# Kernel tuning notes

Measured on AMD Instinct MI355X. Metric: run time of the kernel, lower is better.

## Reference

```python
import jax, jax.numpy as jnp
import numpy as np

B, N, D, H, O = 256, 1024, 512, 2048, 512


def setup_inputs() -> dict:
    key = jax.random.key(0)
    ks = jax.random.split(key, 6)
    x = jax.random.normal(ks[0], (B, N, D), dtype=jnp.float32)
    # binary float mask [B,N,1]; ensure every set has >=1 unpadded element
    mask = (jax.random.uniform(ks[1], (B, N, 1)) < 0.9).astype(jnp.float32)
    mask = mask.at[:, :1, :].set(1.0)
    # per-row (4B rows after stat-concat) unpadded counts in [1, N]
    unpadded = jax.random.randint(ks[2], (4 * B, 1), 1, N + 1).astype(jnp.float32)
    W1 = jax.random.normal(ks[3], (D, H), dtype=jnp.float32) * (1.0 / np.sqrt(D))
    b1 = jnp.zeros((H,), jnp.float32)
    W2 = jax.random.normal(ks[4], (H, O), dtype=jnp.float32) * (1.0 / np.sqrt(H))
    b2 = jnp.zeros((O,), jnp.float32)
    return dict(x=x, mask=mask, unpadded=unpadded, W1=W1, b1=b1, W2=W2, b2=b2)


def reference(x, mask, unpadded, W1, b1, W2, b2):
    # x: [B,N,D], mask: [B,N,1] (0/1 float)
    neg_inf = jnp.float32(-jnp.inf)
    cnt = mask.sum(axis=1)                              # [B,1]
    mean = (x * mask).sum(axis=1) / cnt                 # [B,D]
    agg_max = jnp.where(mask > 0, x, neg_inf).max(axis=1)   # [B,D]
    agg_min = -jnp.where(mask > 0, -x, neg_inf).max(axis=1) # [B,D]
    var = (jnp.square(x - mean[:, None, :]) * mask).sum(axis=1) / cnt
    std = jnp.sqrt(var)                                 # [B,D]
    aggr = jnp.concatenate([mean, agg_max, agg_min, std], axis=0)  # [4B,D]
    # faithful to source: delta = sum(unpadded)/unpadded.shape[1] + 1 (scalar)
    delta = unpadded.sum() / unpadded.shape[1] + 1.0
    logu = jnp.log(unpadded + 1.0)                      # [4B,1]
    amplification = aggr * (logu / delta)
    attenuation = aggr * (delta / logu)
    scale_concat = jnp.concatenate([aggr, amplification, attenuation], axis=0)  # [12B,D]
    h = jax.nn.relu(scale_concat @ W1 + b1)
    return h @ W2 + b2                                  # [12B,O]
```

## Files before the change

kernel.cpp:

```cpp
#include <hip/hip_runtime.h>
#include <hip/hip_bf16.h>
#include <math.h>
#include <stdint.h>

#define B_  256
#define N_  1024
#define D_  512
#define H_  2048
#define O_  512
#define M4  (4 * B_)
#define M12 (12 * B_)
#define NCH 8

typedef __attribute__((ext_vector_type(8))) short short8;
typedef __attribute__((ext_vector_type(4))) float f32x4;
typedef unsigned short ushort_t;

__device__ inline uint32_t pkbf(float a, float b) {
    union { __hip_bfloat162 h; uint32_t u; } cv;
    cv.h = __float22bfloat162_rn(float2{a, b});
    return cv.u;
}
__device__ inline ushort_t f2bf(float f) {
    union { float f; uint32_t u; } v; v.f = f;
    uint32_t r = v.u + 0x7FFFu + ((v.u >> 16) & 1u);
    return (ushort_t)(r >> 16);
}

__device__ inline void load_lds16(const void* g, void* l) {
    typedef const __attribute__((address_space(1))) uint32_t* gp_t;
    typedef __attribute__((address_space(3))) uint32_t* lp_t;
    __builtin_amdgcn_global_load_lds((gp_t)(uintptr_t)g, (lp_t)(uint32_t)(uintptr_t)l,
                                     16, 0, 0);
}

__device__ __forceinline__ void agg_core(const float* __restrict__ x,
                                         const float* __restrict__ mask,
                                         float* __restrict__ part,
                                         float* __restrict__ cntp,
                                         int id, int t) {
    const int b    = id >> 2;
    const int c    = id & 3;
    const int half = t >> 7;
    const int d4   = (t & 127) << 2;
    const float* base = x + ((size_t)b * N_ + (size_t)c * 256) * D_ + d4;
    const float* mp   = mask + (size_t)b * N_ + (size_t)c * 256;

    f32x4 sum = {0.f,0.f,0.f,0.f}, sq = {0.f,0.f,0.f,0.f};
    f32x4 mx = {-INFINITY,-INFINITY,-INFINITY,-INFINITY};
    f32x4 mn = { INFINITY, INFINITY, INFINITY, INFINITY};
    float cnt = 0.f;

    #pragma unroll 8
    for (int n = half; n < 256; n += 2) {
        float m = mp[n];
        f32x4 v = __builtin_nontemporal_load((const f32x4*)(base + (size_t)n * D_));
        sum.x = fmaf(v.x, m, sum.x); sum.y = fmaf(v.y, m, sum.y);
        sum.z = fmaf(v.z, m, sum.z); sum.w = fmaf(v.w, m, sum.w);
        sq.x  = fmaf(v.x * v.x, m, sq.x); sq.y = fmaf(v.y * v.y, m, sq.y);
        sq.z  = fmaf(v.z * v.z, m, sq.z); sq.w = fmaf(v.w * v.w, m, sq.w);
        cnt  += m;
        bool um = m > 0.f;
        mx.x = um ? fmaxf(mx.x, v.x) : mx.x; mx.y = um ? fmaxf(mx.y, v.y) : mx.y;
        mx.z = um ? fmaxf(mx.z, v.z) : mx.z; mx.w = um ? fmaxf(mx.w, v.w) : mx.w;
        mn.x = um ? fminf(mn.x, v.x) : mn.x; mn.y = um ? fminf(mn.y, v.y) : mn.y;
        mn.z = um ? fminf(mn.z, v.z) : mn.z; mn.w = um ? fminf(mn.w, v.w) : mn.w;
    }

    const int ch = c * 2 + half;
    const size_t SS = (size_t)B_ * NCH * D_;
    const size_t pi = ((size_t)(b * NCH + ch)) * D_ + d4;
    *(f32x4*)(part + 0 * SS + pi) = sum;
    *(f32x4*)(part + 1 * SS + pi) = sq;
    *(f32x4*)(part + 2 * SS + pi) = mx;
    *(f32x4*)(part + 3 * SS + pi) = mn;
    if ((t & 127) == 0) cntp[b * NCH + ch] = cnt;
}

__device__ void conv_tile(const float* __restrict__ in, ushort_t* __restrict__ out,
                          int R, int C, int bx, int by, float* tile) {
    const int t  = threadIdx.x;
    const int r0 = by << 5;
    const int c0 = bx << 5;
    const int tr = t >> 3;
    const int tc = (t & 7) << 2;

    float4 v = *(const float4*)(in + (size_t)(r0 + tr) * C + c0 + tc);
    tile[tr * 33 + tc + 0] = v.x; tile[tr * 33 + tc + 1] = v.y;
    tile[tr * 33 + tc + 2] = v.z; tile[tr * 33 + tc + 3] = v.w;
    __syncthreads();

    union { uint32_t u[2]; ushort4 us; } o;
    o.u[0] = pkbf(tile[(tc + 0) * 33 + tr], tile[(tc + 1) * 33 + tr]);
    o.u[1] = pkbf(tile[(tc + 2) * 33 + tr], tile[(tc + 3) * 33 + tr]);
    *(ushort4*)(out + (size_t)(c0 + tr) * R + r0 + tc) = o.us;
}

__global__ __launch_bounds__(256) void k1_mega(const float* __restrict__ x,
                                               const float* __restrict__ mask,
                                               const float* __restrict__ W1,
                                               const float* __restrict__ W2,
                                               const float* __restrict__ unpadded,
                                               float* __restrict__ part,
                                               float* __restrict__ cntp,
                                               ushort_t* __restrict__ W1t,
                                               ushort_t* __restrict__ W2t,
                                               float* __restrict__ scale) {
    __shared__ float smem[32 * 33];
    const int id = blockIdx.x;
    const int t  = threadIdx.x;

    if (id < 1024) {
        agg_core(x, mask, part, cntp, id, t);
    } else if (id < 2048) {
        const int tid = id - 1024;
        conv_tile(W1, W1t, D_, H_, tid & 63, tid >> 6, smem);
    } else if (id < 3072) {
        const int tid = id - 2048;
        conv_tile(W2, W2t, H_, O_, tid & 15, tid >> 4, smem);
    } else {
        float4 u4 = *(const float4*)(unpadded + t * 4);
        smem[t] = u4.x + u4.y + u4.z + u4.w;
        __syncthreads();
        for (int s = 128; s > 0; s >>= 1) {
            if (t < s) smem[t] += smem[t + s];
            __syncthreads();
        }
        const float delta = smem[0] + 1.0f;
        float uu[4] = {u4.x, u4.y, u4.z, u4.w};
        #pragma unroll
        for (int j = 0; j < 4; ++j) {
            const int i = t * 4 + j;
            const float logu = logf(uu[j] + 1.0f);
            scale[i]          = 1.0f;
            scale[M4 + i]     = logu / delta;
            scale[2 * M4 + i] = delta / logu;
        }
    }
}

__global__ __launch_bounds__(256) void agg_final(const float* __restrict__ part,
                                                 const float* __restrict__ cntp,
                                                 ushort_t* __restrict__ aggr) {
    const int b = blockIdx.x;
    const int t = threadIdx.x;
    const int d = 2 * t;

    float cnt = 0.f;
    #pragma unroll
    for (int c = 0; c < NCH; ++c) cnt += cntp[b * NCH + c];

    const size_t SS = (size_t)B_ * NCH * D_;
    float2 sum = {0.f, 0.f}, sq = {0.f, 0.f};
    float2 mx = {-INFINITY, -INFINITY}, mn = {INFINITY, INFINITY};
    #pragma unroll
    for (int c = 0; c < NCH; ++c) {
        const size_t pi = ((size_t)(b * NCH + c)) * D_ + d;
        float2 s  = *(const float2*)(part + 0 * SS + pi);
        float2 q  = *(const float2*)(part + 1 * SS + pi);
        float2 vx = *(const float2*)(part + 2 * SS + pi);
        float2 vn = *(const float2*)(part + 3 * SS + pi);
        sum.x += s.x; sum.y += s.y;
        sq.x  += q.x; sq.y  += q.y;
        mx.x = fmaxf(mx.x, vx.x); mx.y = fmaxf(mx.y, vx.y);
        mn.x = fminf(mn.x, vn.x); mn.y = fminf(mn.y, vn.y);
    }
    const float ic = 1.f / cnt;
    float2 mean = {sum.x * ic, sum.y * ic};
    float2 var  = {fmaxf(sq.x * ic - mean.x * mean.x, 0.f),
                   fmaxf(sq.y * ic - mean.y * mean.y, 0.f)};

    *(uint32_t*)(aggr + (size_t)(0 * B_ + b) * D_ + d) = pkbf(mean.x, mean.y);
    *(uint32_t*)(aggr + (size_t)(1 * B_ + b) * D_ + d) = pkbf(mx.x, mx.y);
    *(uint32_t*)(aggr + (size_t)(2 * B_ + b) * D_ + d) = pkbf(mn.x, mn.y);
    *(uint32_t*)(aggr + (size_t)(3 * B_ + b) * D_ + d) = pkbf(sqrtf(var.x), sqrtf(var.y));
}

__global__ __launch_bounds__(256) void gemm1_h(const ushort_t* __restrict__ A,
                                               const ushort_t* __restrict__ Bt,
                                               const float* __restrict__ scale,
                                               const float* __restrict__ b1,
                                               ushort_t* __restrict__ h) {
    __shared__ ushort_t As0[64 * 64], As1[64 * 64];
    __shared__ ushort_t Bs0[64 * 64], Bs1[64 * 64];

    const int t    = threadIdx.x;
    const int wave = t >> 6;
    const int lane = t & 63;
    const int wm   = wave >> 1, wn = wave & 1;
    const int row0 = blockIdx.y << 6;
    const int col0 = blockIdx.x << 6;

    const int lr  = lane >> 3;
    const int ksw = ((lane & 7) ^ lr) << 3;

    const int rl = lane & 15;
    const int hi = lane >> 4;

    const ushort_t* Ag0 = A  + (size_t)(row0 + wave * 8 + lr) * D_ + ksw;
    const ushort_t* Ag1 = A  + (size_t)(row0 + 32 + wave * 8 + lr) * D_ + ksw;
    const ushort_t* Bg0 = Bt + (size_t)(col0 + wave * 8 + lr) * D_ + ksw;
    const ushort_t* Bg1 = Bt + (size_t)(col0 + 32 + wave * 8 + lr) * D_ + ksw;
    const int ld0 = (wave * 8) * 64;
    const int ld1 = (32 + wave * 8) * 64;

    f32x4 acc[2][2] = {};

    ushort_t* Ac = As0; ushort_t* An = As1;
    ushort_t* Bc = Bs0; ushort_t* Bn = Bs1;

    load_lds16(Ag0, Ac + ld0); load_lds16(Ag1, Ac + ld1);
    load_lds16(Bg0, Bc + ld0); load_lds16(Bg1, Bc + ld1);
    __syncthreads();

    for (int tt = 0; tt < D_ / 64; ++tt) {
        const int k1 = (tt + 1) * 64;
        if (tt + 1 < D_ / 64) {
            load_lds16(Ag0 + k1, An + ld0); load_lds16(Ag1 + k1, An + ld1);
            load_lds16(Bg0 + k1, Bn + ld0); load_lds16(Bg1 + k1, Bn + ld1);
        }
        short8 av[2][2], bv[2][2];
        #pragma unroll
        for (int i = 0; i < 2; ++i) {
            const int ra = wm * 32 + i * 16 + rl;
            const int rb = wn * 32 + i * 16 + rl;
            #pragma unroll
            for (int k2 = 0; k2 < 2; ++k2) {
                av[i][k2] = *(const short8*)(Ac + ra * 64 + (((k2 * 4 + hi) ^ (ra & 7)) << 3));
                bv[i][k2] = *(const short8*)(Bc + rb * 64 + (((k2 * 4 + hi) ^ (rb & 7)) << 3));
            }
        }
        #pragma unroll
        for (int i = 0; i < 2; ++i)
            #pragma unroll
            for (int j = 0; j < 2; ++j)
                #pragma unroll
                for (int k2 = 0; k2 < 2; ++k2)
                    acc[i][j] = __builtin_amdgcn_mfma_f32_16x16x32_bf16(av[i][k2], bv[j][k2], acc[i][j], 0, 0, 0);
        __syncthreads();
        ushort_t* tp;
        tp = Ac; Ac = An; An = tp;
        tp = Bc; Bc = Bn; Bn = tp;
    }

    #pragma unroll
    for (int i = 0; i < 2; ++i) {
        #pragma unroll
        for (int v = 0; v < 4; ++v) {
            const int row = row0 + wm * 32 + i * 16 + hi * 4 + v;
            const float s1 = scale[M4 + row];
            const float s2 = scale[2 * M4 + row];
            #pragma unroll
            for (int j = 0; j < 2; ++j) {
                const int col = col0 + wn * 32 + j * 16 + rl;
                const float bb = b1[col];
                const float z  = acc[i][j][v];
                h[(size_t)row * H_ + col]            = f2bf(fmaxf(z + bb, 0.f));
                h[(size_t)(M4 + row) * H_ + col]     = f2bf(fmaxf(fmaf(s1, z, bb), 0.f));
                h[(size_t)(2 * M4 + row) * H_ + col] = f2bf(fmaxf(fmaf(s2, z, bb), 0.f));
            }
        }
    }
}

__global__ __launch_bounds__(512) void gemm2_pure(const ushort_t* __restrict__ h,
                                                  const ushort_t* __restrict__ W2t,
                                                  const float* __restrict__ b2,
                                                  float* __restrict__ out) {
    __shared__ ushort_t As[2][2][64 * 64];
    __shared__ ushort_t Bs[2][2][64 * 64];

    const int t    = threadIdx.x;
    const int wave = t >> 6;
    const int kg   = wave >> 2;
    const int w4   = wave & 3;
    const int lane = t & 63;
    const int wm   = w4 >> 1, wn = w4 & 1;

    const int id  = blockIdx.x;
    const int xcd = id & 7;
    const int idx = id >> 3;
    const int rb  = xcd * 6 + (idx % 6);
    const int cb  = idx / 6;
    const int row0 = rb << 6;
    const int col0 = cb << 6;

    const int lr  = lane >> 3;
    const int ksw = ((lane & 7) ^ lr) << 3;
    const int kbase = kg * (H_ / 2);

    const ushort_t* Ag0 = h   + (size_t)(row0 + w4 * 8 + lr) * H_ + kbase + ksw;
    const ushort_t* Ag1 = h   + (size_t)(row0 + 32 + w4 * 8 + lr) * H_ + kbase + ksw;
    const ushort_t* Bg0 = W2t + (size_t)(col0 + w4 * 8 + lr) * H_ + kbase + ksw;
    const ushort_t* Bg1 = W2t + (size_t)(col0 + 32 + w4 * 8 + lr) * H_ + kbase + ksw;
    const int ld0 = (w4 * 8) * 64;
    const int ld1 = (32 + w4 * 8) * 64;

    const int rl = lane & 15;
    const int hi = lane >> 4;

    f32x4 acc[2][2] = {};

    ushort_t* Ac = &As[kg][0][0]; ushort_t* An = &As[kg][1][0];
    ushort_t* Bc = &Bs[kg][0][0]; ushort_t* Bn = &Bs[kg][1][0];

    load_lds16(Ag0, Ac + ld0); load_lds16(Ag1, Ac + ld1);
    load_lds16(Bg0, Bc + ld0); load_lds16(Bg1, Bc + ld1);
    __syncthreads();

    for (int tt = 0; tt < 16; ++tt) {
        const int k1 = (tt + 1) * 64;
        if (tt + 1 < 16) {
            load_lds16(Ag0 + k1, An + ld0); load_lds16(Ag1 + k1, An + ld1);
            load_lds16(Bg0 + k1, Bn + ld0); load_lds16(Bg1 + k1, Bn + ld1);
        }
        short8 av[2][2], bv[2][2];
        #pragma unroll
        for (int i = 0; i < 2; ++i) {
            const int ra = wm * 32 + i * 16 + rl;
            const int rb2 = wn * 32 + i * 16 + rl;
            #pragma unroll
            for (int k2 = 0; k2 < 2; ++k2) {
                av[i][k2] = *(const short8*)(Ac + ra * 64 + (((k2 * 4 + hi) ^ (ra & 7)) << 3));
                bv[i][k2] = *(const short8*)(Bc + rb2 * 64 + (((k2 * 4 + hi) ^ (rb2 & 7)) << 3));
            }
        }
        #pragma unroll
        for (int i = 0; i < 2; ++i)
            #pragma unroll
            for (int j = 0; j < 2; ++j)
                #pragma unroll
                for (int k2 = 0; k2 < 2; ++k2)
                    acc[i][j] = __builtin_amdgcn_mfma_f32_16x16x32_bf16(av[i][k2], bv[j][k2], acc[i][j], 0, 0, 0);
        __syncthreads();
        ushort_t* tp;
        tp = Ac; Ac = An; An = tp;
        tp = Bc; Bc = Bn; Bn = tp;
    }

    float* red = (float*)&As[0][0][0];
    const int fidx = w4 * 1024 + lane * 16;
    if (kg == 1) {
        #pragma unroll
        for (int i = 0; i < 2; ++i)
            #pragma unroll
            for (int j = 0; j < 2; ++j)
                #pragma unroll
                for (int v = 0; v < 4; ++v)
                    red[fidx + i * 8 + j * 4 + v] = acc[i][j][v];
    }
    __syncthreads();
    if (kg == 0) {
        #pragma unroll
        for (int i = 0; i < 2; ++i)
            #pragma unroll
            for (int j = 0; j < 2; ++j) {
                const int col = col0 + wn * 32 + j * 16 + rl;
                const float bb = b2[col];
                #pragma unroll
                for (int v = 0; v < 4; ++v) {
                    const int row = row0 + wm * 32 + i * 16 + hi * 4 + v;
                    out[(size_t)row * O_ + col] =
                        acc[i][j][v] + red[fidx + i * 8 + j * 4 + v] + bb;
                }
            }
    }
}

extern "C" void kernel_launch(void* const* d_in, const int* in_sizes, int n_in,
                              void* d_out, int out_size, void* d_ws, size_t ws_size,
                              hipStream_t stream) {
    const float* x        = (const float*)d_in[0];
    const float* mask     = (const float*)d_in[1];
    const float* unpadded = (const float*)d_in[2];
    const float* W1       = (const float*)d_in[3];
    const float* b1       = (const float*)d_in[4];
    const float* W2       = (const float*)d_in[5];
    const float* b2       = (const float*)d_in[6];
    float* out = (float*)d_out;

    float* ws = (float*)d_ws;
    float* part  = ws;
    float* cntp  = ws + 4194304;
    float* scale = ws + 4196352;
    ushort_t* bfw  = (ushort_t*)(ws + 4200448);
    ushort_t* W1t  = bfw;
    ushort_t* W2t  = bfw + 1048576;
    ushort_t* aggr = bfw + 2097152;
    ushort_t* h    = bfw + 2621440;

    k1_mega<<<3073, 256, 0, stream>>>(x, mask, W1, W2, unpadded,
                                      part, cntp, W1t, W2t, scale);
    agg_final<<<B_, 256, 0, stream>>>(part, cntp, aggr);
    gemm1_h<<<dim3(H_ / 64, M4 / 64), 256, 0, stream>>>(aggr, W1t, scale, b1, h);
    gemm2_pure<<<384, 512, 0, stream>>>(h, W2t, b2, out);
}
```

Before: 126.4 us.

## Fuse set aggregation finalization into first kernel via in-block LDS reduction

Each block now reduces half of the feature columns over the full set of 1024 rows for one batch element. The four waves' partial sum, sum-of-squares, max, min and count are combined in LDS, and the bf16 aggregates are written directly. This removes the partials buffer round trip through global memory and the separate agg_final launch. In exchange there are half as many aggregation blocks (512 instead of 1024), each doing twice the streaming work, which may reduce the memory parallelism available for reading x.

```diff
diff --git a/kernel.cpp b/kernel.cpp
--- a/kernel.cpp
+++ b/kernel.cpp
@@ -10,7 +10,6 @@
 #define O_  512
 #define M4  (4 * B_)
 #define M12 (12 * B_)
-#define NCH 8
 
 typedef __attribute__((ext_vector_type(8))) short short8;
 typedef __attribute__((ext_vector_type(4))) float f32x4;
@@ -32,49 +31,6 @@
     typedef __attribute__((address_space(3))) uint32_t* lp_t;
     __builtin_amdgcn_global_load_lds((gp_t)(uintptr_t)g, (lp_t)(uint32_t)(uintptr_t)l,
                                      16, 0, 0);
-}
-
-__device__ __forceinline__ void agg_core(const float* __restrict__ x,
-                                         const float* __restrict__ mask,
-                                         float* __restrict__ part,
-                                         float* __restrict__ cntp,
-                                         int id, int t) {
-    const int b    = id >> 2;
-    const int c    = id & 3;
-    const int half = t >> 7;
-    const int d4   = (t & 127) << 2;
-    const float* base = x + ((size_t)b * N_ + (size_t)c * 256) * D_ + d4;
-    const float* mp   = mask + (size_t)b * N_ + (size_t)c * 256;
-
-    f32x4 sum = {0.f,0.f,0.f,0.f}, sq = {0.f,0.f,0.f,0.f};
-    f32x4 mx = {-INFINITY,-INFINITY,-INFINITY,-INFINITY};
-    f32x4 mn = { INFINITY, INFINITY, INFINITY, INFINITY};
-    float cnt = 0.f;
-
-    #pragma unroll 8
-    for (int n = half; n < 256; n += 2) {
-        float m = mp[n];
-        f32x4 v = __builtin_nontemporal_load((const f32x4*)(base + (size_t)n * D_));
-        sum.x = fmaf(v.x, m, sum.x); sum.y = fmaf(v.y, m, sum.y);
-        sum.z = fmaf(v.z, m, sum.z); sum.w = fmaf(v.w, m, sum.w);
-        sq.x  = fmaf(v.x * v.x, m, sq.x); sq.y = fmaf(v.y * v.y, m, sq.y);
-        sq.z  = fmaf(v.z * v.z, m, sq.z); sq.w = fmaf(v.w * v.w, m, sq.w);
-        cnt  += m;
-        bool um = m > 0.f;
-        mx.x = um ? fmaxf(mx.x, v.x) : mx.x; mx.y = um ? fmaxf(mx.y, v.y) : mx.y;
-        mx.z = um ? fmaxf(mx.z, v.z) : mx.z; mx.w = um ? fmaxf(mx.w, v.w) : mx.w;
-        mn.x = um ? fminf(mn.x, v.x) : mn.x; mn.y = um ? fminf(mn.y, v.y) : mn.y;
-        mn.z = um ? fminf(mn.z, v.z) : mn.z; mn.w = um ? fminf(mn.w, v.w) : mn.w;
-    }
-
-    const int ch = c * 2 + half;
-    const size_t SS = (size_t)B_ * NCH * D_;
-    const size_t pi = ((size_t)(b * NCH + ch)) * D_ + d4;
-    *(f32x4*)(part + 0 * SS + pi) = sum;
-    *(f32x4*)(part + 1 * SS + pi) = sq;
-    *(f32x4*)(part + 2 * SS + pi) = mx;
-    *(f32x4*)(part + 3 * SS + pi) = mn;
-    if ((t & 127) == 0) cntp[b * NCH + ch] = cnt;
 }
 
 __device__ void conv_tile(const float* __restrict__ in, ushort_t* __restrict__ out,
@@ -101,24 +57,97 @@
                                                const float* __restrict__ W1,
                                                const float* __restrict__ W2,
                                                const float* __restrict__ unpadded,
-                                               float* __restrict__ part,
-                                               float* __restrict__ cntp,
                                                ushort_t* __restrict__ W1t,
                                                ushort_t* __restrict__ W2t,
-                                               float* __restrict__ scale) {
-    __shared__ float smem[32 * 33];
+                                               float* __restrict__ scale,
+                                               ushort_t* __restrict__ aggr) {
+    __shared__ char smem_raw[16448];
     const int id = blockIdx.x;
     const int t  = threadIdx.x;
 
-    if (id < 1024) {
-        agg_core(x, mask, part, cntp, id, t);
-    } else if (id < 2048) {
-        const int tid = id - 1024;
-        conv_tile(W1, W1t, D_, H_, tid & 63, tid >> 6, smem);
-    } else if (id < 3072) {
-        const int tid = id - 2048;
-        conv_tile(W2, W2t, H_, O_, tid & 15, tid >> 4, smem);
+    if (id < 512) {
+        const int b    = id >> 1;
+        const int half = id & 1;
+        const int wv   = t >> 6;
+        const int lane = t & 63;
+        const int d    = half * 256 + lane * 4;
+        const float* base = x + (size_t)b * N_ * D_ + d;
+        const float* mp   = mask + (size_t)b * N_;
+
+        f32x4 sum = {0.f,0.f,0.f,0.f}, sq = {0.f,0.f,0.f,0.f};
+        f32x4 mx = {-INFINITY,-INFINITY,-INFINITY,-INFINITY};
+        f32x4 mn = { INFINITY, INFINITY, INFINITY, INFINITY};
+        float cnt = 0.f;
+
+        #pragma unroll 8
+        for (int n = wv; n < N_; n += 4) {
+            float m = mp[n];
+            f32x4 v = __builtin_nontemporal_load((const f32x4*)(base + (size_t)n * D_));
+            sum.x = fmaf(v.x, m, sum.x); sum.y = fmaf(v.y, m, sum.y);
+            sum.z = fmaf(v.z, m, sum.z); sum.w = fmaf(v.w, m, sum.w);
+            sq.x  = fmaf(v.x * v.x, m, sq.x); sq.y = fmaf(v.y * v.y, m, sq.y);
+            sq.z  = fmaf(v.z * v.z, m, sq.z); sq.w = fmaf(v.w * v.w, m, sq.w);
+            cnt  += m;
+            bool um = m > 0.f;
+            mx.x = um ? fmaxf(mx.x, v.x) : mx.x; mx.y = um ? fmaxf(mx.y, v.y) : mx.y;
+            mx.z = um ? fmaxf(mx.z, v.z) : mx.z; mx.w = um ? fmaxf(mx.w, v.w) : mx.w;
+            mn.x = um ? fminf(mn.x, v.x) : mn.x; mn.y = um ? fminf(mn.y, v.y) : mn.y;
+            mn.z = um ? fminf(mn.z, v.z) : mn.z; mn.w = um ? fminf(mn.w, v.w) : mn.w;
+        }
+
+        f32x4* Lsum = (f32x4*)(smem_raw);
+        f32x4* Lsq  = (f32x4*)(smem_raw + 4096);
+        f32x4* Lmx  = (f32x4*)(smem_raw + 8192);
+        f32x4* Lmn  = (f32x4*)(smem_raw + 12288);
+        float* Lc   = (float*)(smem_raw + 16384);
+        Lsum[wv * 64 + lane] = sum;
+        Lsq [wv * 64 + lane] = sq;
+        Lmx [wv * 64 + lane] = mx;
+        Lmn [wv * 64 + lane] = mn;
+        if (lane == 0) Lc[wv] = cnt;
+        __syncthreads();
+
+        if (wv == 0) {
+            #pragma unroll
+            for (int w = 1; w < 4; ++w) {
+                f32x4 s = Lsum[w * 64 + lane];
+                f32x4 q = Lsq [w * 64 + lane];
+                f32x4 X = Lmx [w * 64 + lane];
+                f32x4 M = Lmn [w * 64 + lane];
+                sum.x += s.x; sum.y += s.y; sum.z += s.z; sum.w += s.w;
+                sq.x  += q.x; sq.y  += q.y; sq.z  += q.z; sq.w  += q.w;
+                mx.x = fmaxf(mx.x, X.x); mx.y = fmaxf(mx.y, X.y);
+                mx.z = fmaxf(mx.z, X.z); mx.w = fmaxf(mx.w, X.w);
+                mn.x = fminf(mn.x, M.x); mn.y = fminf(mn.y, M.y);
+                mn.z = fminf(mn.z, M.z); mn.w = fminf(mn.w, M.w);
+            }
+            const float c  = Lc[0] + Lc[1] + Lc[2] + Lc[3];
+            const float ic = 1.f / c;
+            f32x4 mean = {sum.x * ic, sum.y * ic, sum.z * ic, sum.w * ic};
+            f32x4 var  = {fmaxf(sq.x * ic - mean.x * mean.x, 0.f),
+                          fmaxf(sq.y * ic - mean.y * mean.y, 0.f),
+                          fmaxf(sq.z * ic - mean.z * mean.z, 0.f),
+                          fmaxf(sq.w * ic - mean.w * mean.w, 0.f)};
+
+            union { uint32_t u[2]; ushort4 us; } o;
+            o.u[0] = pkbf(mean.x, mean.y); o.u[1] = pkbf(mean.z, mean.w);
+            *(ushort4*)(aggr + (size_t)(0 * B_ + b) * D_ + d) = o.us;
+            o.u[0] = pkbf(mx.x, mx.y); o.u[1] = pkbf(mx.z, mx.w);
+            *(ushort4*)(aggr + (size_t)(1 * B_ + b) * D_ + d) = o.us;
+            o.u[0] = pkbf(mn.x, mn.y); o.u[1] = pkbf(mn.z, mn.w);
+            *(ushort4*)(aggr + (size_t)(2 * B_ + b) * D_ + d) = o.us;
+            o.u[0] = pkbf(sqrtf(var.x), sqrtf(var.y));
+            o.u[1] = pkbf(sqrtf(var.z), sqrtf(var.w));
+            *(ushort4*)(aggr + (size_t)(3 * B_ + b) * D_ + d) = o.us;
+        }
+    } else if (id < 1536) {
+        const int tid = id - 512;
+        conv_tile(W1, W1t, D_, H_, tid & 63, tid >> 6, (float*)smem_raw);
+    } else if (id < 2560) {
+        const int tid = id - 1536;
+        conv_tile(W2, W2t, H_, O_, tid & 15, tid >> 4, (float*)smem_raw);
     } else {
+        float* smem = (float*)smem_raw;
         float4 u4 = *(const float4*)(unpadded + t * 4);
         smem[t] = u4.x + u4.y + u4.z + u4.w;
         __syncthreads();
@@ -137,43 +166,6 @@
             scale[2 * M4 + i] = delta / logu;
         }
     }
-}
-
-__global__ __launch_bounds__(256) void agg_final(const float* __restrict__ part,
-                                                 const float* __restrict__ cntp,
-                                                 ushort_t* __restrict__ aggr) {
-    const int b = blockIdx.x;
-    const int t = threadIdx.x;
-    const int d = 2 * t;
-
-    float cnt = 0.f;
-    #pragma unroll
-    for (int c = 0; c < NCH; ++c) cnt += cntp[b * NCH + c];
-
-    const size_t SS = (size_t)B_ * NCH * D_;
-    float2 sum = {0.f, 0.f}, sq = {0.f, 0.f};
-    float2 mx = {-INFINITY, -INFINITY}, mn = {INFINITY, INFINITY};
-    #pragma unroll
-    for (int c = 0; c < NCH; ++c) {
-        const size_t pi = ((size_t)(b * NCH + c)) * D_ + d;
-        float2 s  = *(const float2*)(part + 0 * SS + pi);
-        float2 q  = *(const float2*)(part + 1 * SS + pi);
-        float2 vx = *(const float2*)(part + 2 * SS + pi);
-        float2 vn = *(const float2*)(part + 3 * SS + pi);
-        sum.x += s.x; sum.y += s.y;
-        sq.x  += q.x; sq.y  += q.y;
-        mx.x = fmaxf(mx.x, vx.x); mx.y = fmaxf(mx.y, vx.y);
-        mn.x = fminf(mn.x, vn.x); mn.y = fminf(mn.y, vn.y);
-    }
-    const float ic = 1.f / cnt;
-    float2 mean = {sum.x * ic, sum.y * ic};
-    float2 var  = {fmaxf(sq.x * ic - mean.x * mean.x, 0.f),
-                   fmaxf(sq.y * ic - mean.y * mean.y, 0.f)};
-
-    *(uint32_t*)(aggr + (size_t)(0 * B_ + b) * D_ + d) = pkbf(mean.x, mean.y);
-    *(uint32_t*)(aggr + (size_t)(1 * B_ + b) * D_ + d) = pkbf(mx.x, mx.y);
-    *(uint32_t*)(aggr + (size_t)(2 * B_ + b) * D_ + d) = pkbf(mn.x, mn.y);
-    *(uint32_t*)(aggr + (size_t)(3 * B_ + b) * D_ + d) = pkbf(sqrtf(var.x), sqrtf(var.y));
 }
 
 __global__ __launch_bounds__(256) void gemm1_h(const ushort_t* __restrict__ A,
@@ -380,18 +372,15 @@
     float* out = (float*)d_out;
 
     float* ws = (float*)d_ws;
-    float* part  = ws;
-    float* cntp  = ws + 4194304;
-    float* scale = ws + 4196352;
-    ushort_t* bfw  = (ushort_t*)(ws + 4200448);
+    float* scale = ws;
+    ushort_t* bfw  = (ushort_t*)(ws + 4096);
     ushort_t* W1t  = bfw;
     ushort_t* W2t  = bfw + 1048576;
     ushort_t* aggr = bfw + 2097152;
     ushort_t* h    = bfw + 2621440;
 
-    k1_mega<<<3073, 256, 0, stream>>>(x, mask, W1, W2, unpadded,
-                                      part, cntp, W1t, W2t, scale);
-    agg_final<<<B_, 256, 0, stream>>>(part, cntp, aggr);
+    k1_mega<<<2561, 256, 0, stream>>>(x, mask, W1, W2, unpadded,
+                                      W1t, W2t, scale, aggr);
     gemm1_h<<<dim3(H_ / 64, M4 / 64), 256, 0, stream>>>(aggr, W1t, scale, b1, h);
     gemm2_pure<<<384, 512, 0, stream>>>(h, W2t, b2, out);
 }
```

Measured after the change: 113.6 us. -10.1%, faster.
